# Optimization experiments

Hardware: AMD Instinct MI355X
Metric: run time of the kernel (lower is better)

The kernel has to match this reference:

```python
import jax, jax.numpy as jnp
import numpy as np

N = 50000   # total nodes across batched graphs
E = 800000  # total edges
F = 30      # input node features
G = 256     # number of graphs in the disjoint batch
CH = [128, 64, 32]
N_LABELS = 2


def setup_inputs() -> dict:
    key = jax.random.key(0)
    ks = jax.random.split(key, 16)
    x = jax.random.normal(ks[0], (N, F), dtype=jnp.float32)
    edge_weight = jax.random.uniform(ks[1], (E,), dtype=jnp.float32)
    edge_row = jax.random.randint(ks[2], (E,), 0, N, dtype=jnp.int32)
    edge_col = jax.random.randint(ks[3], (E,), 0, N, dtype=jnp.int32)
    seg = jnp.sort(jax.random.randint(ks[4], (N,), 0, G, dtype=jnp.int32))
    # GCSConv params: out = A @ (x W1) + x W2 + b, per layer
    dims = [F] + CH
    params = {}
    kk = 5
    for l in range(3):
        fin, fout = dims[l], dims[l + 1]
        s = 1.0 / np.sqrt(fin)
        params[f"w1_{l+1}"] = jax.random.uniform(ks[kk], (fin, fout), minval=-s, maxval=s, dtype=jnp.float32); kk += 1
        params[f"w2_{l+1}"] = jax.random.uniform(ks[kk], (fin, fout), minval=-s, maxval=s, dtype=jnp.float32); kk += 1
        params[f"b_{l+1}"] = jnp.zeros((fout,), dtype=jnp.float32)
    sd = 1.0 / np.sqrt(CH[-1])
    params["wd"] = jax.random.uniform(ks[kk], (CH[-1], N_LABELS), minval=-sd, maxval=sd, dtype=jnp.float32)
    params["bd"] = jnp.zeros((N_LABELS,), dtype=jnp.float32)
    return {"x": x, "edge_weight": edge_weight, "edge_row": edge_row,
            "edge_col": edge_col, "seg": seg, **params}


def _gcs_conv(x, ew, er, ec, w1, w2, b):
    # spektral GCSConv: relu(A @ (x W1) + x W2 + b) with sparse A in COO form
    h = x @ w1                                   # [N, Fout]
    msgs = ew[:, None] * h[ec]                   # gather along edges [E, Fout]
    agg = jax.ops.segment_sum(msgs, er, num_segments=N)  # SpMM scatter [N, Fout]
    return jax.nn.relu(agg + x @ w2 + b)


def reference(x, edge_weight, edge_row, edge_col, seg,
              w1_1, w2_1, b_1, w1_2, w2_2, b_2, w1_3, w2_3, b_3, wd, bd):
    h = _gcs_conv(x, edge_weight, edge_row, edge_col, w1_1, w2_1, b_1)
    h = _gcs_conv(h, edge_weight, edge_row, edge_col, w1_2, w2_2, b_2)
    h = _gcs_conv(h, edge_weight, edge_row, edge_col, w1_3, w2_3, b_3)
    # GlobalAvgPool: segment mean over graph ids
    sums = jax.ops.segment_sum(h, seg, num_segments=G)               # [G, 32]
    cnts = jax.ops.segment_sum(jnp.ones((N,), h.dtype), seg, num_segments=G)
    pooled = sums / jnp.maximum(cnts, 1.0)[:, None]
    return jax.nn.softmax(pooled @ wd + bd, axis=-1)                 # [G, 2]
```

## Files before the change

kernel.cpp:

```cpp
#include <hip/hip_runtime.h>
#include <hip/hip_fp16.h>

#define N_NODES 50000
#define N_EDGES 800000
#define N_GRAPHS 256
#define NCB 196
#define CHUNK 3125
#define MBLK 782

typedef _Float16 f16x8 __attribute__((ext_vector_type(8)));
typedef float    f32x4 __attribute__((ext_vector_type(4)));

__global__ __launch_bounds__(256)
void hist_prep(const int* __restrict__ ER, const float* __restrict__ X,
               const int* __restrict__ SEG,
               const float* __restrict__ W1, const float* __restrict__ W2,
               const float* __restrict__ W12, const float* __restrict__ W22,
               const float* __restrict__ W13, const float* __restrict__ W23,
               int* __restrict__ ghist, __half* __restrict__ XPh,
               int* __restrict__ start,
               __half* __restrict__ W1f, __half* __restrict__ W2f,
               __half* __restrict__ W3f)
{
    int b = blockIdx.x;
    int t = threadIdx.x;
    if (b < 256) {
        __shared__ int h[NCB];
        for (int i = t; i < NCB; i += 256) h[i] = 0;
        __syncthreads();
        int lo = b * CHUNK, hi = lo + CHUNK;
        for (int e = lo + t; e < hi; e += 256) atomicAdd(&h[ER[e] >> 8], 1);
        __syncthreads();
        for (int i = t; i < NCB; i += 256) ghist[i * 256 + b] = h[i];
        return;
    }
    int bid = b - 256;
    if (bid < 782) {
        int idx = bid * 256 + t;
        int n = idx >> 2;
        int c4 = idx & 3;
        if (n >= N_NODES) return;
        __half2 hb[4];
        #pragma unroll
        for (int k = 0; k < 4; ++k) {
            int c0 = c4 * 8 + 2 * k;
            float v0 = (c0 < 30) ? X[n * 30 + c0] : 0.f;
            float v1 = (c0 + 1 < 30) ? X[n * 30 + c0 + 1] : 0.f;
            hb[k] = __float22half2_rn(make_float2(v0, v1));
        }
        *(uint4*)(XPh + (size_t)n * 32 + c4 * 8) = *(uint4*)&hb[0];
    } else if (bid < 978) {
        int n = (bid - 782) * 256 + t;
        if (n >= N_NODES) return;
        int g = SEG[n];
        int gprev = (n == 0) ? -1 : SEG[n - 1];
        for (int gg = gprev + 1; gg <= g; ++gg) start[gg] = n;
        if (n == N_NODES - 1)
            for (int gg = g + 1; gg <= N_GRAPHS; ++gg) start[gg] = N_NODES;
    } else {
        int idx = (bid - 978) * 256 + t;
        if (idx < 8192) {
            int i = idx & 7, c = (idx >> 3) & 15, g = (idx >> 7) & 3;
            int s = (idx >> 9) & 1, n = idx >> 10;
            int k = s * 32 + g * 8 + i, col = n * 16 + c;
            float w = 0.f;
            if (k < 30) w = W1[k * 128 + col];
            else if (k >= 32 && k < 62) w = W2[(k - 32) * 128 + col];
            W1f[idx] = __float2half(w);
        } else if (idx < 24576) {
            int o = idx - 8192;
            int i = o & 7, c = (o >> 3) & 15, g = (o >> 7) & 3;
            int s = (o >> 9) & 3, n = o >> 11;
            int k = s * 32 + g * 8 + i, col = n * 16 + c;
            float w = (col < 64) ? W12[k * 64 + col] : W22[k * 64 + col - 64];
            W2f[o] = __float2half(w);
        } else {
            int o = idx - 24576;
            int i = o & 7, c = (o >> 3) & 15, g = (o >> 7) & 3;
            int s = (o >> 9) & 1, n = o >> 10;
            int k = s * 32 + g * 8 + i, col = n * 16 + c;
            float w = (col < 32) ? W13[k * 32 + col] : W23[k * 32 + col - 32];
            W3f[o] = __float2half(w);
        }
    }
}

__global__ __launch_bounds__(256)
void scan1(int* __restrict__ ghist, int* __restrict__ bsum)
{
    __shared__ int s[256];
    int t = threadIdx.x, b = blockIdx.x;
    int i = b * 256 + t;
    int v = ghist[i];
    s[t] = v;
    __syncthreads();
    for (int off = 1; off < 256; off <<= 1) {
        int u = (t >= off) ? s[t - off] : 0;
        __syncthreads();
        s[t] += u;
        __syncthreads();
    }
    ghist[i] = s[t] - v;
    if (t == 255) bsum[b] = s[255];
}

__global__ __launch_bounds__(1024)
void c_scatter(const int* __restrict__ ER, const int* __restrict__ EC,
               const float* __restrict__ EW, const int* __restrict__ ghist,
               const int* __restrict__ bsum, uint2* __restrict__ tmp)
{
    __shared__ int s[256];
    __shared__ int cur[NCB];
    int t = threadIdx.x, blk = blockIdx.x;
    int v = 0;
    if (t < 256) {
        v = (t < NCB) ? bsum[t] : 0;
        s[t] = v;
    }
    __syncthreads();
    for (int off = 1; off < 256; off <<= 1) {
        int u = 0;
        if (t < 256 && t >= off) u = s[t - off];
        __syncthreads();
        if (t < 256) s[t] += u;
        __syncthreads();
    }
    if (t < NCB) cur[t] = (s[t] - v) + ghist[t * 256 + blk];
    __syncthreads();
    int lo = blk * CHUNK, hi = lo + CHUNK;
    for (int e = lo + t; e < hi; e += 1024) {
        int d = ER[e];
        int pos = atomicAdd(&cur[d >> 8], 1);
        tmp[pos] = make_uint2((unsigned int)EC[e] | ((unsigned int)(d & 255) << 16),
                              (unsigned int)__half_as_ushort(__float2half(EW[e])));
    }
}

__device__ __forceinline__ void fma8h(float4& a0, float4& a1, float w,
                                      const uint4& raw)
{
    const __half2* hp = (const __half2*)&raw;
    float2 f0 = __half22float2(hp[0]);
    float2 f1 = __half22float2(hp[1]);
    float2 f2 = __half22float2(hp[2]);
    float2 f3 = __half22float2(hp[3]);
    a0.x = fmaf(w, f0.x, a0.x); a0.y = fmaf(w, f0.y, a0.y);
    a0.z = fmaf(w, f1.x, a0.z); a0.w = fmaf(w, f1.y, a0.w);
    a1.x = fmaf(w, f2.x, a1.x); a1.y = fmaf(w, f2.y, a1.y);
    a1.z = fmaf(w, f3.x, a1.z); a1.w = fmaf(w, f3.y, a1.w);
}

__global__ __launch_bounds__(1024)
void bsort(const uint2* __restrict__ tmp, const int* __restrict__ bsum,
           unsigned int* __restrict__ packed, int* __restrict__ rowptr)
{
    __shared__ int s[256];
    __shared__ int hist[256];
    __shared__ int cur[256];
    int t = threadIdx.x, b = blockIdx.x;

    if (t < 256) s[t] = (t < NCB) ? bsum[t] : 0;
    __syncthreads();
    for (int off = 1; off < 256; off <<= 1) {
        int u = 0;
        if (t < 256 && t >= off) u = s[t - off];
        __syncthreads();
        if (t < 256) s[t] += u;
        __syncthreads();
    }
    int cntb = bsum[b];
    int base = s[b] - cntb;
    int end  = base + cntb;
    __syncthreads();

    if (t < 256) hist[t] = 0;
    __syncthreads();
    for (int j = base + t; j < end; j += 1024)
        atomicAdd(&hist[(tmp[j].x >> 16) & 255], 1);
    __syncthreads();
    int hv = 0;
    if (t < 256) { hv = hist[t]; s[t] = hv; }
    __syncthreads();
    for (int off = 1; off < 256; off <<= 1) {
        int u = 0;
        if (t < 256 && t >= off) u = s[t - off];
        __syncthreads();
        if (t < 256) s[t] += u;
        __syncthreads();
    }
    if (t < 256) {
        int excl = s[t] - hv;
        int n = b * 256 + t;
        if (n < N_NODES) rowptr[n] = base + excl;
        if (b == NCB - 1 && t == 0) rowptr[N_NODES] = N_EDGES;
        cur[t] = base + excl;
    }
    __syncthreads();
    for (int j = base + t; j < end; j += 1024) {
        uint2 v = tmp[j];
        int pos = atomicAdd(&cur[(v.x >> 16) & 255], 1);
        packed[pos] = (v.x & 0xFFFF) | (v.y << 16);
    }
}

__global__ __launch_bounds__(512)
void dense12_mfma(const __half* __restrict__ XPh, const int* __restrict__ rowptr,
                  const unsigned int* __restrict__ packed,
                  const __half* __restrict__ W1f, const float* __restrict__ B1,
                  const __half* __restrict__ W2f, const float* __restrict__ B2,
                  __half* __restrict__ H2h, __half* __restrict__ A2h)
{
    __shared__ __align__(16) __half As[64 * 72];
    __shared__ __align__(16) __half Hs[64 * 136];
    const int tid = threadIdx.x;
    const int m0 = blockIdx.x * 64;

    if (tid < 256) {
        int row = tid >> 2, c4 = tid & 3;
        int gm = m0 + row;
        uint4 v = make_uint4(0, 0, 0, 0);
        if (gm < N_NODES) v = *(const uint4*)(XPh + (size_t)gm * 32 + c4 * 8);
        *(uint4*)(As + row * 72 + (4 + c4) * 8) = v;
    }
    {
        int local = tid >> 3;
        int es = (tid >> 2) & 1;
        int q = tid & 3;
        int n = m0 + local;
        float4 acc0 = make_float4(0.f, 0.f, 0.f, 0.f);
        float4 acc1 = make_float4(0.f, 0.f, 0.f, 0.f);
        if (n < N_NODES) {
            int r0 = rowptr[n], r1 = rowptr[n + 1];
            int mid = (r0 + r1) >> 1;
            int lo = es ? mid : r0;
            int hi = es ? r1 : mid;
            int j = lo;
            for (; j + 3 < hi; j += 4) {
                unsigned int ra = packed[j],     rb = packed[j + 1];
                unsigned int rc = packed[j + 2], rd = packed[j + 3];
                uint4 rawa = *(const uint4*)(XPh + (size_t)(ra & 0xFFFF) * 32 + q * 8);
                uint4 rawb = *(const uint4*)(XPh + (size_t)(rb & 0xFFFF) * 32 + q * 8);
                uint4 rawc = *(const uint4*)(XPh + (size_t)(rc & 0xFFFF) * 32 + q * 8);
                uint4 rawd = *(const uint4*)(XPh + (size_t)(rd & 0xFFFF) * 32 + q * 8);
                float wa = __half2float(__ushort_as_half((unsigned short)(ra >> 16)));
                float wb = __half2float(__ushort_as_half((unsigned short)(rb >> 16)));
                float wc = __half2float(__ushort_as_half((unsigned short)(rc >> 16)));
                float wd = __half2float(__ushort_as_half((unsigned short)(rd >> 16)));
                fma8h(acc0, acc1, wa, rawa);
                fma8h(acc0, acc1, wb, rawb);
                fma8h(acc0, acc1, wc, rawc);
                fma8h(acc0, acc1, wd, rawd);
            }
            for (; j < hi; ++j) {
                unsigned int r = packed[j];
                uint4 raw = *(const uint4*)(XPh + (size_t)(r & 0xFFFF) * 32 + q * 8);
                float wv = __half2float(__ushort_as_half((unsigned short)(r >> 16)));
                fma8h(acc0, acc1, wv, raw);
            }
        }
        float* part = (float*)Hs;
        if (es == 1) {
            *(float4*)&part[local * 36 + q * 8 + 0] = acc0;
            *(float4*)&part[local * 36 + q * 8 + 4] = acc1;
        }
        __syncthreads();
        if (es == 0) {
            float4 p0 = *(float4*)&part[local * 36 + q * 8 + 0];
            float4 p1 = *(float4*)&part[local * 36 + q * 8 + 4];
            acc0.x += p0.x; acc0.y += p0.y; acc0.z += p0.z; acc0.w += p0.w;
            acc1.x += p1.x; acc1.y += p1.y; acc1.z += p1.z; acc1.w += p1.w;
            __half2 hb2[4];
            hb2[0] = __float22half2_rn(make_float2(acc0.x, acc0.y));
            hb2[1] = __float22half2_rn(make_float2(acc0.z, acc0.w));
            hb2[2] = __float22half2_rn(make_float2(acc1.x, acc1.y));
            hb2[3] = __float22half2_rn(make_float2(acc1.z, acc1.w));
            *(uint4*)(As + local * 72 + q * 8) = *(uint4*)&hb2[0];
        }
    }
    __syncthreads();

    const int lane = tid & 63;
    const int w  = tid >> 6;
    const int lr = lane & 15;
    const int lg = lane >> 4;

    f32x4 acc[4];
    #pragma unroll
    for (int m = 0; m < 4; ++m) acc[m] = (f32x4){0.f, 0.f, 0.f, 0.f};

    #pragma unroll
    for (int s = 0; s < 2; ++s) {
        f16x8 b = *(const f16x8*)(W1f + (((w * 2 + s) * 4 + lg) * 16 + lr) * 8);
        #pragma unroll
        for (int m = 0; m < 4; ++m) {
            f16x8 a = *(const f16x8*)(As + (m * 16 + lr) * 72 + s * 32 + lg * 8);
            acc[m] = __builtin_amdgcn_mfma_f32_16x16x32_f16(a, b, acc[m], 0, 0, 0);
        }
    }

    {
        const float bias = B1[w * 16 + lr];
        #pragma unroll
        for (int m = 0; m < 4; ++m)
            #pragma unroll
            for (int r = 0; r < 4; ++r) {
                float v = fmaxf(acc[m][r] + bias, 0.f);
                Hs[(m * 16 + lg * 4 + r) * 136 + w * 16 + lr] = __float2half(v);
            }
    }
    __syncthreads();

    f32x4 acc2[4];
    #pragma unroll
    for (int m = 0; m < 4; ++m) acc2[m] = (f32x4){0.f, 0.f, 0.f, 0.f};

    #pragma unroll
    for (int s = 0; s < 4; ++s) {
        f16x8 b = *(const f16x8*)(W2f + (((w * 4 + s) * 4 + lg) * 16 + lr) * 8);
        #pragma unroll
        for (int m = 0; m < 4; ++m) {
            f16x8 a = *(const f16x8*)(Hs + (m * 16 + lr) * 136 + s * 32 + lg * 8);
            acc2[m] = __builtin_amdgcn_mfma_f32_16x16x32_f16(a, b, acc2[m], 0, 0, 0);
        }
    }
    __syncthreads();

    {
        const float bias = (w >= 4) ? B2[(w - 4) * 16 + lr] : 0.f;
        #pragma unroll
        for (int m = 0; m < 4; ++m)
            #pragma unroll
            for (int r = 0; r < 4; ++r)
                Hs[(m * 16 + lg * 4 + r) * 136 + w * 16 + lr] =
                    __float2half(acc2[m][r] + bias);
    }
    __syncthreads();

    for (int idx = tid; idx < 1024; idx += 512) {
        int row = idx >> 4, c8 = idx & 15;
        int gm = m0 + row;
        if (gm < N_NODES) {
            uint4 v = *(const uint4*)(Hs + row * 136 + c8 * 8);
            if (c8 < 8) *(uint4*)(H2h + (size_t)gm * 64 + c8 * 8) = v;
            else        *(uint4*)(A2h + (size_t)gm * 64 + (c8 - 8) * 8) = v;
        }
    }
}

__global__ __launch_bounds__(1024)
void spmm_dense3(const __half* __restrict__ H2h, const int* __restrict__ rowptr,
                 const unsigned int* __restrict__ packed,
                 const __half* __restrict__ A2h, const __half* __restrict__ W3f,
                 const float* __restrict__ B3, __half* __restrict__ H3h,
                 __half* __restrict__ B2h)
{
    __shared__ __align__(16) __half As[64 * 72];
    __shared__ __align__(16) __half Os[64 * 72];
    __shared__ float part[64][68];
    const int tid = threadIdx.x;
    const int m0 = blockIdx.x * 64;

    {
        int local = tid >> 4;
        int es = (tid >> 3) & 1;
        int q = tid & 7;
        int n = m0 + local;
        float4 acc0 = make_float4(0.f, 0.f, 0.f, 0.f);
        float4 acc1 = make_float4(0.f, 0.f, 0.f, 0.f);
        if (n < N_NODES) {
            int r0 = rowptr[n], r1 = rowptr[n + 1];
            int mid = (r0 + r1) >> 1;
            int lo = es ? mid : r0;
            int hi = es ? r1 : mid;
            if (es == 0) {
                uint4 raw = *(const uint4*)(A2h + (size_t)n * 64 + q * 8);
                const __half2* hp = (const __half2*)&raw;
                float2 f0 = __half22float2(hp[0]);
                float2 f1 = __half22float2(hp[1]);
                float2 f2 = __half22float2(hp[2]);
                float2 f3 = __half22float2(hp[3]);
                acc0 = make_float4(f0.x, f0.y, f1.x, f1.y);
                acc1 = make_float4(f2.x, f2.y, f3.x, f3.y);
            }
            int j = lo;
            for (; j + 3 < hi; j += 4) {
                unsigned int ra = packed[j],     rb = packed[j + 1];
                unsigned int rc = packed[j + 2], rd = packed[j + 3];
                uint4 rawa = *(const uint4*)(H2h + (size_t)(ra & 0xFFFF) * 64 + q * 8);
                uint4 rawb = *(const uint4*)(H2h + (size_t)(rb & 0xFFFF) * 64 + q * 8);
                uint4 rawc = *(const uint4*)(H2h + (size_t)(rc & 0xFFFF) * 64 + q * 8);
                uint4 rawd = *(const uint4*)(H2h + (size_t)(rd & 0xFFFF) * 64 + q * 8);
                float wa = __half2float(__ushort_as_half((unsigned short)(ra >> 16)));
                float wb = __half2float(__ushort_as_half((unsigned short)(rb >> 16)));
                float wc = __half2float(__ushort_as_half((unsigned short)(rc >> 16)));
                float wd = __half2float(__ushort_as_half((unsigned short)(rd >> 16)));
                fma8h(acc0, acc1, wa, rawa);
                fma8h(acc0, acc1, wb, rawb);
                fma8h(acc0, acc1, wc, rawc);
                fma8h(acc0, acc1, wd, rawd);
            }
            for (; j < hi; ++j) {
                unsigned int r = packed[j];
                uint4 raw = *(const uint4*)(H2h + (size_t)(r & 0xFFFF) * 64 + q * 8);
                float w = __half2float(__ushort_as_half((unsigned short)(r >> 16)));
                fma8h(acc0, acc1, w, raw);
            }
        }
        if (es == 1) {
            *(float4*)&part[local][q * 8 + 0] = acc0;
            *(float4*)&part[local][q * 8 + 4] = acc1;
        }
        __syncthreads();
        if (es == 0) {
            float4 p0 = *(float4*)&part[local][q * 8 + 0];
            float4 p1 = *(float4*)&part[local][q * 8 + 4];
            acc0.x += p0.x; acc0.y += p0.y; acc0.z += p0.z; acc0.w += p0.w;
            acc1.x += p1.x; acc1.y += p1.y; acc1.z += p1.z; acc1.w += p1.w;
            __half2 hb[4];
            hb[0] = __float22half2_rn(make_float2(fmaxf(acc0.x, 0.f), fmaxf(acc0.y, 0.f)));
            hb[1] = __float22half2_rn(make_float2(fmaxf(acc0.z, 0.f), fmaxf(acc0.w, 0.f)));
            hb[2] = __float22half2_rn(make_float2(fmaxf(acc1.x, 0.f), fmaxf(acc1.y, 0.f)));
            hb[3] = __float22half2_rn(make_float2(fmaxf(acc1.z, 0.f), fmaxf(acc1.w, 0.f)));
            *(uint4*)(As + local * 72 + q * 8) = *(uint4*)&hb[0];
        }
    }
    __syncthreads();

    const int lane = tid & 63;
    const int w  = tid >> 6;
    const int wm = w >> 2;
    const int wn = w & 3;
    const int lr = lane & 15;
    const int lg = lane >> 4;

    f32x4 acc = (f32x4){0.f, 0.f, 0.f, 0.f};
    #pragma unroll
    for (int s = 0; s < 2; ++s) {
        f16x8 b = *(const f16x8*)(W3f + (((wn * 2 + s) * 4 + lg) * 16 + lr) * 8);
        f16x8 a = *(const f16x8*)(As + (wm * 16 + lr) * 72 + s * 32 + lg * 8);
        acc = __builtin_amdgcn_mfma_f32_16x16x32_f16(a, b, acc, 0, 0, 0);
    }

    const float bias = (wn >= 2) ? B3[(wn - 2) * 16 + lr] : 0.f;
    #pragma unroll
    for (int r = 0; r < 4; ++r)
        Os[(wm * 16 + lg * 4 + r) * 72 + wn * 16 + lr] = __float2half(acc[r] + bias);
    __syncthreads();

    if (tid < 512) {
        int row = tid >> 3, c8 = tid & 7;
        int gm = m0 + row;
        if (gm < N_NODES) {
            uint4 v = *(const uint4*)(Os + row * 72 + c8 * 8);
            if (c8 < 4) *(uint4*)(H3h + (size_t)gm * 32 + c8 * 8) = v;
            else        *(uint4*)(B2h + (size_t)gm * 32 + (c8 - 4) * 8) = v;
        }
    }
}

template<int FOUT, int S>
__global__ __launch_bounds__(512)
void spmm_split(const __half* __restrict__ H, const int* __restrict__ rowptr,
                const unsigned int* __restrict__ packed, __half* __restrict__ AGGh)
{
    constexpr int T = FOUT / 8;
    constexpr int NPB = 512 / (S * T);
    __shared__ float part[NPB][S - 1][FOUT + 4];
    int tid = threadIdx.x;
    int local = tid / (S * T);
    int rem = tid % (S * T);
    int s = rem / T;
    int q = rem % T;
    int n = blockIdx.x * NPB + local;
    bool valid = (n < N_NODES);
    float4 acc0 = make_float4(0.f, 0.f, 0.f, 0.f);
    float4 acc1 = make_float4(0.f, 0.f, 0.f, 0.f);
    __half* ap = AGGh + (size_t)n * FOUT + q * 8;
    if (valid) {
        int r0 = rowptr[n], r1 = rowptr[n + 1];
        int deg = r1 - r0;
        int lo = r0 + (deg * s) / S;
        int hi = r0 + (deg * (s + 1)) / S;
        if (s == 0) {
            uint4 raw = *(const uint4*)ap;
            const __half2* hp = (const __half2*)&raw;
            float2 f0 = __half22float2(hp[0]);
            float2 f1 = __half22float2(hp[1]);
            float2 f2 = __half22float2(hp[2]);
            float2 f3 = __half22float2(hp[3]);
            acc0 = make_float4(f0.x, f0.y, f1.x, f1.y);
            acc1 = make_float4(f2.x, f2.y, f3.x, f3.y);
        }
        int j = lo;
        for (; j + 3 < hi; j += 4) {
            unsigned int ra = packed[j],     rb = packed[j + 1];
            unsigned int rc = packed[j + 2], rd = packed[j + 3];
            uint4 rawa = *(const uint4*)(H + (size_t)(ra & 0xFFFF) * FOUT + q * 8);
            uint4 rawb = *(const uint4*)(H + (size_t)(rb & 0xFFFF) * FOUT + q * 8);
            uint4 rawc = *(const uint4*)(H + (size_t)(rc & 0xFFFF) * FOUT + q * 8);
            uint4 rawd = *(const uint4*)(H + (size_t)(rd & 0xFFFF) * FOUT + q * 8);
            float wa = __half2float(__ushort_as_half((unsigned short)(ra >> 16)));
            float wb = __half2float(__ushort_as_half((unsigned short)(rb >> 16)));
            float wc = __half2float(__ushort_as_half((unsigned short)(rc >> 16)));
            float wd = __half2float(__ushort_as_half((unsigned short)(rd >> 16)));
            fma8h(acc0, acc1, wa, rawa);
            fma8h(acc0, acc1, wb, rawb);
            fma8h(acc0, acc1, wc, rawc);
            fma8h(acc0, acc1, wd, rawd);
        }
        for (; j < hi; ++j) {
            unsigned int r = packed[j];
            uint4 raw = *(const uint4*)(H + (size_t)(r & 0xFFFF) * FOUT + q * 8);
            float w = __half2float(__ushort_as_half((unsigned short)(r >> 16)));
            fma8h(acc0, acc1, w, raw);
        }
    }
    if (s > 0) {
        *(float4*)&part[local][s - 1][q * 8 + 0] = acc0;
        *(float4*)&part[local][s - 1][q * 8 + 4] = acc1;
    }
    __syncthreads();
    if (s == 0 && valid) {
        #pragma unroll
        for (int ss = 0; ss < S - 1; ++ss) {
            float4 p0 = *(float4*)&part[local][ss][q * 8 + 0];
            float4 p1 = *(float4*)&part[local][ss][q * 8 + 4];
            acc0.x += p0.x; acc0.y += p0.y; acc0.z += p0.z; acc0.w += p0.w;
            acc1.x += p1.x; acc1.y += p1.y; acc1.z += p1.z; acc1.w += p1.w;
        }
        __half2 hb[4];
        hb[0] = __float22half2_rn(make_float2(acc0.x, acc0.y));
        hb[1] = __float22half2_rn(make_float2(acc0.z, acc0.w));
        hb[2] = __float22half2_rn(make_float2(acc1.x, acc1.y));
        hb[3] = __float22half2_rn(make_float2(acc1.z, acc1.w));
        *(uint4*)ap = *(uint4*)&hb[0];
    }
}

__global__ __launch_bounds__(1024)
void pool_kernel(const __half* __restrict__ H, const int* __restrict__ start,
                 const float* __restrict__ WD, const float* __restrict__ BD,
                 float* __restrict__ OUT)
{
    __shared__ float red[32][33];
    int g = blockIdx.x;
    int s = start[g], e = start[g + 1];
    int q = threadIdx.x & 31;
    int grp = threadIdx.x >> 5;
    float acc = 0.f;
    for (int n = s + grp; n < e; n += 32)
        acc += fmaxf(__half2float(H[(size_t)n * 32 + q]), 0.f);
    red[grp][q] = acc;
    __syncthreads();
    if (threadIdx.x < 32) {
        float v = 0.f;
        #pragma unroll
        for (int i = 0; i < 32; ++i) v += red[i][q];
        float inv = (e > s) ? 1.0f / (float)(e - s) : 1.0f;
        float p = v * inv;
        float p0 = p * WD[q * 2 + 0];
        float p1 = p * WD[q * 2 + 1];
        #pragma unroll
        for (int off = 16; off; off >>= 1) {
            p0 += __shfl_down(p0, off, 32);
            p1 += __shfl_down(p1, off, 32);
        }
        if (q == 0) {
            float l0 = p0 + BD[0], l1 = p1 + BD[1];
            float m = fmaxf(l0, l1);
            float e0 = expf(l0 - m), e1 = expf(l1 - m);
            float si = 1.0f / (e0 + e1);
            OUT[g * 2 + 0] = e0 * si;
            OUT[g * 2 + 1] = e1 * si;
        }
    }
}

extern "C" void kernel_launch(void* const* d_in, const int* in_sizes, int n_in,
                              void* d_out, int out_size, void* d_ws, size_t ws_size,
                              hipStream_t stream)
{
    const float* x    = (const float*)d_in[0];
    const float* ew   = (const float*)d_in[1];
    const int*   er   = (const int*)d_in[2];
    const int*   ec   = (const int*)d_in[3];
    const int*   seg  = (const int*)d_in[4];
    const float* w1_1 = (const float*)d_in[5];
    const float* w2_1 = (const float*)d_in[6];
    const float* b_1  = (const float*)d_in[7];
    const float* w1_2 = (const float*)d_in[8];
    const float* w2_2 = (const float*)d_in[9];
    const float* b_2  = (const float*)d_in[10];
    const float* w1_3 = (const float*)d_in[11];
    const float* w2_3 = (const float*)d_in[12];
    const float* b_3  = (const float*)d_in[13];
    const float* wd   = (const float*)d_in[14];
    const float* bd   = (const float*)d_in[15];

    float* ws = (float*)d_ws;
    int*   IW = (int*)d_ws;
    __half* XPh    = (__half*)ws;
    uint2*  tmp    = (uint2*)(ws + 1600000);
    __half* H2h    = (__half*)(ws + 3200000);
    __half* A2h    = (__half*)(ws + 4800000);
    __half* H3h    = (__half*)(ws + 6400000);
    __half* B2h    = (__half*)(ws + 7200000);
    unsigned int* packed = (unsigned int*)(IW + 8000000);
    int*    rowptr = IW + 9000000;
    int*    ghist  = IW + 9060000;
    int*    bsum   = IW + 9115000;
    int*    start  = IW + 9120000;
    __half* W1f    = (__half*)(ws + 9125000);
    __half* W2f    = (__half*)(ws + 9130000);
    __half* W3f    = (__half*)(ws + 9139000);

    dim3 blk(256);

    hist_prep<<<dim3(256 + 782 + 196 + 112), blk, 0, stream>>>(
        er, x, seg, w1_1, w2_1, w1_2, w2_2, w1_3, w2_3,
        ghist, XPh, start, W1f, W2f, W3f);
    scan1<<<dim3(NCB), blk, 0, stream>>>(ghist, bsum);
    c_scatter<<<dim3(256), dim3(1024), 0, stream>>>(er, ec, ew, ghist, bsum, tmp);
    bsort<<<dim3(NCB), dim3(1024), 0, stream>>>(tmp, bsum, packed, rowptr);

    dense12_mfma<<<dim3(MBLK), dim3(512), 0, stream>>>(XPh, rowptr, packed,
                                                       W1f, b_1, W2f, b_2,
                                                       H2h, A2h);
    spmm_dense3<<<dim3(MBLK), dim3(1024), 0, stream>>>(H2h, rowptr, packed, A2h,
                                                       W3f, b_3, H3h, B2h);
    spmm_split<32, 4><<<dim3((N_NODES + 31) / 32), dim3(512), 0, stream>>>(H3h, rowptr,
                                                                           packed, B2h);

    pool_kernel<<<dim3(N_GRAPHS), dim3(1024), 0, stream>>>(B2h, start, wd, bd,
                                                           (float*)d_out);
}
```

Before: 163.4 us.

## Use 1024-thread blocks: four-way edge split in layer-1 SpMM and 2D wave tiling

The fused layer-1/2 kernel goes from 512 to 1024 threads. Each node's edge list is now split across four thread groups instead of two, with partial sums reduced through a dedicated shared buffer. The MFMA phases use a 2x8 wave grid, so each wave computes two M tiles instead of four. The prep kernel is also relaunched with 1024-thread blocks and correspondingly fewer blocks. The aim is more memory-level parallelism in the gather and more waves to hide latency, at the cost of extra shared memory and a longer reduction step.

Result: no change. 163.8 us (+0.2%).

```diff
diff --git a/kernel.cpp b/kernel.cpp
--- a/kernel.cpp
+++ b/kernel.cpp
@@ -11,7 +11,7 @@
 typedef _Float16 f16x8 __attribute__((ext_vector_type(8)));
 typedef float    f32x4 __attribute__((ext_vector_type(4)));
 
-__global__ __launch_bounds__(256)
+__global__ __launch_bounds__(1024)
 void hist_prep(const int* __restrict__ ER, const float* __restrict__ X,
                const int* __restrict__ SEG,
                const float* __restrict__ W1, const float* __restrict__ W2,
@@ -26,17 +26,17 @@
     int t = threadIdx.x;
     if (b < 256) {
         __shared__ int h[NCB];
-        for (int i = t; i < NCB; i += 256) h[i] = 0;
+        for (int i = t; i < NCB; i += 1024) h[i] = 0;
         __syncthreads();
         int lo = b * CHUNK, hi = lo + CHUNK;
-        for (int e = lo + t; e < hi; e += 256) atomicAdd(&h[ER[e] >> 8], 1);
-        __syncthreads();
-        for (int i = t; i < NCB; i += 256) ghist[i * 256 + b] = h[i];
+        for (int e = lo + t; e < hi; e += 1024) atomicAdd(&h[ER[e] >> 8], 1);
+        __syncthreads();
+        for (int i = t; i < NCB; i += 1024) ghist[i * 256 + b] = h[i];
         return;
     }
     int bid = b - 256;
-    if (bid < 782) {
-        int idx = bid * 256 + t;
+    if (bid < 196) {
+        int idx = bid * 1024 + t;
         int n = idx >> 2;
         int c4 = idx & 3;
         if (n >= N_NODES) return;
@@ -49,8 +49,8 @@
             hb[k] = __float22half2_rn(make_float2(v0, v1));
         }
         *(uint4*)(XPh + (size_t)n * 32 + c4 * 8) = *(uint4*)&hb[0];
-    } else if (bid < 978) {
-        int n = (bid - 782) * 256 + t;
+    } else if (bid < 245) {
+        int n = (bid - 196) * 1024 + t;
         if (n >= N_NODES) return;
         int g = SEG[n];
         int gprev = (n == 0) ? -1 : SEG[n - 1];
@@ -58,7 +58,7 @@
         if (n == N_NODES - 1)
             for (int gg = g + 1; gg <= N_GRAPHS; ++gg) start[gg] = N_NODES;
     } else {
-        int idx = (bid - 978) * 256 + t;
+        int idx = (bid - 245) * 1024 + t;
         if (idx < 8192) {
             int i = idx & 7, c = (idx >> 3) & 15, g = (idx >> 7) & 3;
             int s = (idx >> 9) & 1, n = idx >> 10;
@@ -203,7 +203,7 @@
     }
 }
 
-__global__ __launch_bounds__(512)
+__global__ __launch_bounds__(1024)
 void dense12_mfma(const __half* __restrict__ XPh, const int* __restrict__ rowptr,
                   const unsigned int* __restrict__ packed,
                   const __half* __restrict__ W1f, const float* __restrict__ B1,
@@ -212,6 +212,7 @@
 {
     __shared__ __align__(16) __half As[64 * 72];
     __shared__ __align__(16) __half Hs[64 * 136];
+    __shared__ float part[64][3][36];
     const int tid = threadIdx.x;
     const int m0 = blockIdx.x * 64;
 
@@ -223,17 +224,17 @@
         *(uint4*)(As + row * 72 + (4 + c4) * 8) = v;
     }
     {
-        int local = tid >> 3;
-        int es = (tid >> 2) & 1;
+        int local = tid >> 4;
+        int es = (tid >> 2) & 3;
         int q = tid & 3;
         int n = m0 + local;
         float4 acc0 = make_float4(0.f, 0.f, 0.f, 0.f);
         float4 acc1 = make_float4(0.f, 0.f, 0.f, 0.f);
         if (n < N_NODES) {
             int r0 = rowptr[n], r1 = rowptr[n + 1];
-            int mid = (r0 + r1) >> 1;
-            int lo = es ? mid : r0;
-            int hi = es ? r1 : mid;
+            int deg = r1 - r0;
+            int lo = r0 + (deg * es) / 4;
+            int hi = r0 + (deg * (es + 1)) / 4;
             int j = lo;
             for (; j + 3 < hi; j += 4) {
                 unsigned int ra = packed[j],     rb = packed[j + 1];
@@ -258,17 +259,19 @@
                 fma8h(acc0, acc1, wv, raw);
             }
         }
-        float* part = (float*)Hs;
-        if (es == 1) {
-            *(float4*)&part[local * 36 + q * 8 + 0] = acc0;
-            *(float4*)&part[local * 36 + q * 8 + 4] = acc1;
+        if (es > 0) {
+            *(float4*)&part[local][es - 1][q * 8 + 0] = acc0;
+            *(float4*)&part[local][es - 1][q * 8 + 4] = acc1;
         }
         __syncthreads();
         if (es == 0) {
-            float4 p0 = *(float4*)&part[local * 36 + q * 8 + 0];
-            float4 p1 = *(float4*)&part[local * 36 + q * 8 + 4];
-            acc0.x += p0.x; acc0.y += p0.y; acc0.z += p0.z; acc0.w += p0.w;
-            acc1.x += p1.x; acc1.y += p1.y; acc1.z += p1.z; acc1.w += p1.w;
+            #pragma unroll
+            for (int ss = 0; ss < 3; ++ss) {
+                float4 p0 = *(float4*)&part[local][ss][q * 8 + 0];
+                float4 p1 = *(float4*)&part[local][ss][q * 8 + 4];
+                acc0.x += p0.x; acc0.y += p0.y; acc0.z += p0.z; acc0.w += p0.w;
+                acc1.x += p1.x; acc1.y += p1.y; acc1.z += p1.z; acc1.w += p1.w;
+            }
             __half2 hb2[4];
             hb2[0] = __float22half2_rn(make_float2(acc0.x, acc0.y));
             hb2[1] = __float22half2_rn(make_float2(acc0.z, acc0.w));
@@ -281,63 +284,71 @@
 
     const int lane = tid & 63;
     const int w  = tid >> 6;
+    const int wm = w >> 3;
+    const int wn = w & 7;
     const int lr = lane & 15;
     const int lg = lane >> 4;
 
-    f32x4 acc[4];
-    #pragma unroll
-    for (int m = 0; m < 4; ++m) acc[m] = (f32x4){0.f, 0.f, 0.f, 0.f};
+    f32x4 acc[2];
+    acc[0] = (f32x4){0.f, 0.f, 0.f, 0.f};
+    acc[1] = (f32x4){0.f, 0.f, 0.f, 0.f};
 
     #pragma unroll
     for (int s = 0; s < 2; ++s) {
-        f16x8 b = *(const f16x8*)(W1f + (((w * 2 + s) * 4 + lg) * 16 + lr) * 8);
-        #pragma unroll
-        for (int m = 0; m < 4; ++m) {
-            f16x8 a = *(const f16x8*)(As + (m * 16 + lr) * 72 + s * 32 + lg * 8);
+        f16x8 b = *(const f16x8*)(W1f + (((wn * 2 + s) * 4 + lg) * 16 + lr) * 8);
+        #pragma unroll
+        for (int m = 0; m < 2; ++m) {
+            int mm = wm * 2 + m;
+            f16x8 a = *(const f16x8*)(As + (mm * 16 + lr) * 72 + s * 32 + lg * 8);
             acc[m] = __builtin_amdgcn_mfma_f32_16x16x32_f16(a, b, acc[m], 0, 0, 0);
         }
     }
 
     {
-        const float bias = B1[w * 16 + lr];
-        #pragma unroll
-        for (int m = 0; m < 4; ++m)
+        const float bias = B1[wn * 16 + lr];
+        #pragma unroll
+        for (int m = 0; m < 2; ++m) {
+            int mm = wm * 2 + m;
             #pragma unroll
             for (int r = 0; r < 4; ++r) {
                 float v = fmaxf(acc[m][r] + bias, 0.f);
-                Hs[(m * 16 + lg * 4 + r) * 136 + w * 16 + lr] = __float2half(v);
+                Hs[(mm * 16 + lg * 4 + r) * 136 + wn * 16 + lr] = __float2half(v);
             }
-    }
-    __syncthreads();
-
-    f32x4 acc2[4];
-    #pragma unroll
-    for (int m = 0; m < 4; ++m) acc2[m] = (f32x4){0.f, 0.f, 0.f, 0.f};
+        }
+    }
+    __syncthreads();
+
+    f32x4 acc2[2];
+    acc2[0] = (f32x4){0.f, 0.f, 0.f, 0.f};
+    acc2[1] = (f32x4){0.f, 0.f, 0.f, 0.f};
 
     #pragma unroll
     for (int s = 0; s < 4; ++s) {
-        f16x8 b = *(const f16x8*)(W2f + (((w * 4 + s) * 4 + lg) * 16 + lr) * 8);
-        #pragma unroll
-        for (int m = 0; m < 4; ++m) {
-            f16x8 a = *(const f16x8*)(Hs + (m * 16 + lr) * 136 + s * 32 + lg * 8);
+        f16x8 b = *(const f16x8*)(W2f + (((wn * 4 + s) * 4 + lg) * 16 + lr) * 8);
+        #pragma unroll
+        for (int m = 0; m < 2; ++m) {
+            int mm = wm * 2 + m;
+            f16x8 a = *(const f16x8*)(Hs + (mm * 16 + lr) * 136 + s * 32 + lg * 8);
             acc2[m] = __builtin_amdgcn_mfma_f32_16x16x32_f16(a, b, acc2[m], 0, 0, 0);
         }
     }
     __syncthreads();
 
     {
-        const float bias = (w >= 4) ? B2[(w - 4) * 16 + lr] : 0.f;
-        #pragma unroll
-        for (int m = 0; m < 4; ++m)
+        const float bias = (wn >= 4) ? B2[(wn - 4) * 16 + lr] : 0.f;
+        #pragma unroll
+        for (int m = 0; m < 2; ++m) {
+            int mm = wm * 2 + m;
             #pragma unroll
             for (int r = 0; r < 4; ++r)
-                Hs[(m * 16 + lg * 4 + r) * 136 + w * 16 + lr] =
+                Hs[(mm * 16 + lg * 4 + r) * 136 + wn * 16 + lr] =
                     __float2half(acc2[m][r] + bias);
-    }
-    __syncthreads();
-
-    for (int idx = tid; idx < 1024; idx += 512) {
-        int row = idx >> 4, c8 = idx & 15;
+        }
+    }
+    __syncthreads();
+
+    {
+        int row = tid >> 4, c8 = tid & 15;
         int gm = m0 + row;
         if (gm < N_NODES) {
             uint4 v = *(const uint4*)(Hs + row * 136 + c8 * 8);
@@ -616,16 +627,16 @@
 
     dim3 blk(256);
 
-    hist_prep<<<dim3(256 + 782 + 196 + 112), blk, 0, stream>>>(
+    hist_prep<<<dim3(256 + 196 + 49 + 28), dim3(1024), 0, stream>>>(
         er, x, seg, w1_1, w2_1, w1_2, w2_2, w1_3, w2_3,
         ghist, XPh, start, W1f, W2f, W3f);
     scan1<<<dim3(NCB), blk, 0, stream>>>(ghist, bsum);
     c_scatter<<<dim3(256), dim3(1024), 0, stream>>>(er, ec, ew, ghist, bsum, tmp);
     bsort<<<dim3(NCB), dim3(1024), 0, stream>>>(tmp, bsum, packed, rowptr);
 
-    dense12_mfma<<<dim3(MBLK), dim3(512), 0, stream>>>(XPh, rowptr, packed,
-                                                       W1f, b_1, W2f, b_2,
-                                                       H2h, A2h);
+    dense12_mfma<<<dim3(MBLK), dim3(1024), 0, stream>>>(XPh, rowptr, packed,
+                                                        W1f, b_1, W2f, b_2,
+                                                        H2h, A2h);
     spmm_dense3<<<dim3(MBLK), dim3(1024), 0, stream>>>(H2h, rowptr, packed, A2h,
                                                        W3f, b_3, H3h, B2h);
     spmm_split<32, 4><<<dim3((N_NODES + 31) / 32), dim3(512), 0, stream>>>(H3h, rowptr,
```
